# Kernel optimization log

Measured on AMD Instinct MI355X. Metric: run time of the kernel, lower is better.

The kernel has to match this reference:

```python
import jax, jax.numpy as jnp
import numpy as np

N = 50000
E = 800000
IN_DIM = 128
HID = 64
OUT_DIM = 128
NEG_SLOPE = 0.2  # PyG GATConv default


def _add_self_loops(src, dst, edge_attr, n):
    # PyG GATConv(add_self_loops=True) with edge_dim uses fill_value='mean':
    # self-loop edge_attr = mean of edge_attr of incoming edges per node.
    deg = jax.ops.segment_sum(jnp.ones((src.shape[0],), edge_attr.dtype), dst, num_segments=n)
    loop_attr = jax.ops.segment_sum(edge_attr, dst, num_segments=n) / jnp.maximum(deg, 1.0)[:, None]
    loop = jnp.arange(n, dtype=src.dtype)
    return (jnp.concatenate([src, loop]), jnp.concatenate([dst, loop]),
            jnp.concatenate([edge_attr, loop_attr], axis=0))


def _gat_conv(x, src, dst, edge_attr, W, We, a_src, a_dst, a_edge, bias, heads, out_dim, concat, n):
    src, dst, edge_attr = _add_self_loops(src, dst, edge_attr, n)
    h = (x @ W).reshape(n, heads, out_dim)                      # [N,H,D]
    he = (edge_attr @ We).reshape(-1, heads, out_dim)           # [E',H,D]
    alpha_src = jnp.einsum('nhd,hd->nh', h, a_src)
    alpha_dst = jnp.einsum('nhd,hd->nh', h, a_dst)
    alpha_edge = jnp.einsum('ehd,hd->eh', he, a_edge)
    alpha = jax.nn.leaky_relu(alpha_src[src] + alpha_dst[dst] + alpha_edge, NEG_SLOPE)  # [E',H]
    # segment softmax over edges grouped by destination node
    amax = jax.ops.segment_max(alpha, dst, num_segments=n)
    amax = jnp.where(jnp.isfinite(amax), amax, 0.0)
    ex = jnp.exp(alpha - amax[dst])
    denom = jax.ops.segment_sum(ex, dst, num_segments=n)
    coef = ex / (denom[dst] + 1e-16)                            # [E',H]
    msg = h[src] * coef[:, :, None]                             # [E',H,D]
    out = jax.ops.segment_sum(msg, dst, num_segments=n)         # [N,H,D]
    out = out.reshape(n, heads * out_dim) if concat else out.mean(axis=1)
    return out + bias


def setup_inputs() -> dict:
    key = jax.random.key(0)
    ks = jax.random.split(key, 16)
    s = 0.05
    inp = {
        'x': jax.random.normal(ks[0], (N, IN_DIM), jnp.float32),
        'edge_index': jax.random.randint(ks[1], (2, E), 0, N, dtype=jnp.int64),
        'edge_attr': jax.random.normal(ks[2], (E, 2), jnp.float32),
        # gat1: heads=4, concat -> out 4*HID
        'W1': jax.random.normal(ks[3], (IN_DIM, 4 * HID), jnp.float32) * s,
        'We1': jax.random.normal(ks[4], (2, 4 * HID), jnp.float32) * s,
        'asrc1': jax.random.normal(ks[5], (4, HID), jnp.float32) * s,
        'adst1': jax.random.normal(ks[6], (4, HID), jnp.float32) * s,
        'aedge1': jax.random.normal(ks[7], (4, HID), jnp.float32) * s,
        'b1': jnp.zeros((4 * HID,), jnp.float32),
        # gat2: heads=1, concat=False -> out OUT_DIM
        'W2': jax.random.normal(ks[8], (4 * HID, OUT_DIM), jnp.float32) * s,
        'We2': jax.random.normal(ks[9], (2, OUT_DIM), jnp.float32) * s,
        'asrc2': jax.random.normal(ks[10], (1, OUT_DIM), jnp.float32) * s,
        'adst2': jax.random.normal(ks[11], (1, OUT_DIM), jnp.float32) * s,
        'aedge2': jax.random.normal(ks[12], (1, OUT_DIM), jnp.float32) * s,
        'b2': jnp.zeros((OUT_DIM,), jnp.float32),
    }
    return inp


def reference(x, edge_index, edge_attr, W1, We1, asrc1, adst1, aedge1, b1,
              W2, We2, asrc2, adst2, aedge2, b2):
    src, dst = edge_index[0], edge_index[1]
    # dropout layers are identity in eval mode
    h = _gat_conv(x, src, dst, edge_attr, W1, We1, asrc1, adst1, aedge1, b1,
                  heads=4, out_dim=HID, concat=True, n=x.shape[0])
    h = jax.nn.elu(h)
    out = _gat_conv(h, src, dst, edge_attr, W2, We2, asrc2, adst2, aedge2, b2,
                    heads=1, out_dim=OUT_DIM, concat=False, n=x.shape[0])
    return out
```

## Files before the change

### kernel.cpp

```cpp
#include <hip/hip_runtime.h>
#include <hip/hip_bf16.h>

#define NN 50000
#define EE 800000
#define SCAN_B 2048
#define NB ((NN + SCAN_B - 1) / SCAN_B)
#define LOG2E 1.44269504088896340736f


typedef short bf16x8 __attribute__((ext_vector_type(8)));
typedef float f32x4  __attribute__((ext_vector_type(4)));
typedef float f32x2  __attribute__((ext_vector_type(2)));

__device__ __forceinline__ float bf2f(unsigned short u) {
    return __uint_as_float(((unsigned)u) << 16);
}
__device__ __forceinline__ unsigned short f2bf(float f) {
    unsigned b = __float_as_uint(f);
    b += 0x7fffu + ((b >> 16) & 1u);
    return (unsigned short)(b >> 16);
}
__device__ __forceinline__ float2 bfpair(unsigned u) {
    return make_float2(__uint_as_float(u << 16), __uint_as_float(u & 0xffff0000u));
}
__device__ __forceinline__ f32x2 bfpair2(unsigned u) {
    f32x2 r;
    r.x = __uint_as_float(u << 16);
    r.y = __uint_as_float(u & 0xffff0000u);
    return r;
}

__global__ void k_prep(const float* __restrict__ We1, const float* __restrict__ ae1,
                       const float* __restrict__ We2, const float* __restrict__ ae2,
                       float* __restrict__ v,
                       const float* __restrict__ as1, const float* __restrict__ ad1,
                       float* __restrict__ Asd,
                       const float* __restrict__ W1, unsigned short* __restrict__ W1t,
                       const float* __restrict__ W2, unsigned short* __restrict__ W2t,
                       const int* __restrict__ ei, int* __restrict__ idg,
                       int* __restrict__ rank,
                       const float* __restrict__ x, unsigned short* __restrict__ xb) {
    int bid = blockIdx.x, t = threadIdx.x;
    if (bid == 0) {
        if (t < 8) {
            int c = t >> 2, h = t & 3;
            float s = 0.f;
            for (int d = 0; d < 64; d++) s += We1[c * 256 + h * 64 + d] * ae1[h * 64 + d];
            v[c * 4 + h] = s * LOG2E;
        } else if (t < 10) {
            int c = t - 8;
            float s = 0.f;
            for (int d = 0; d < 128; d++) s += We2[c * 128 + d] * ae2[d];
            v[8 + c] = s * LOG2E;
        }
        #pragma unroll 1
        for (int idx = t; idx < 1024; idx += 256) {
            int k = idx >> 3, j = idx & 7;
            const float* a = (j < 4) ? as1 : ad1;
            int h = j & 3;
            float s = 0.f;
            for (int c = 0; c < 64; c++) s += W1[k * 256 + h * 64 + c] * a[h * 64 + c];
            Asd[idx] = s * LOG2E;
        }
    } else if (bid <= 256) {
        int idx = (bid - 1) * 256 + t;
        if (idx < 32768) {
            int k = idx >> 8, n = idx & 255;
            W1t[n * 128 + k] = f2bf(W1[idx]);
        } else {
            int i = idx - 32768;
            int k = i >> 7, n = i & 127;
            W2t[n * 256 + k] = f2bf(W2[i]);
        }
    } else if (bid <= 256 + 3125) {
        int e = (bid - 257) * 256 + t;
        if (e < EE) rank[e] = atomicAdd(&idg[ei[EE + e]], 1);
    } else {
        int i = (bid - 3382) * 256 + t;
        if (i < NN * 128 / 4) {
            float4 vv = ((const float4*)x)[i];
            ushort4 o;
            o.x = f2bf(vv.x); o.y = f2bf(vv.y); o.z = f2bf(vv.z); o.w = f2bf(vv.w);
            ((ushort4*)xb)[i] = o;
        }
    }
}

__global__ void k_scan1(const int* __restrict__ idg, int* __restrict__ rowptr,
                        int* __restrict__ bsum) {
    __shared__ int sh[512];
    int t = threadIdx.x;
    int base = blockIdx.x * SCAN_B + t * 4;
    int v[4]; int s = 0;
    #pragma unroll
    for (int j = 0; j < 4; j++) {
        int i = base + j;
        v[j] = (i < NN) ? idg[i] : 0;
        s += v[j];
    }
    sh[t] = s;
    __syncthreads();
    for (int off = 1; off < 512; off <<= 1) {
        int a = (t >= off) ? sh[t - off] : 0;
        __syncthreads();
        sh[t] += a;
        __syncthreads();
    }
    int run = sh[t] - s;
    #pragma unroll
    for (int j = 0; j < 4; j++) {
        int i = base + j;
        if (i < NN) rowptr[i] = run;
        run += v[j];
    }
    if (t == 511) bsum[blockIdx.x] = sh[511];
}

__global__ void k_scan2(const int* __restrict__ bsum, int* __restrict__ boff,
                        int* __restrict__ rowptr) {
    if (threadIdx.x == 0) {
        int acc = 0;
        for (int b = 0; b < NB; b++) { boff[b] = acc; acc += bsum[b]; }
        rowptr[NN] = acc;
    }
}

__global__ void k_scan3(int* __restrict__ rowptr, const int* __restrict__ boff) {
    int t = threadIdx.x;
    int i = blockIdx.x * SCAN_B + t * 4;
    int off = boff[blockIdx.x];
    #pragma unroll
    for (int j = 0; j < 4; j++)
        if (i + j < NN) rowptr[i + j] += off;
}

__global__ void k_scatter(const int* __restrict__ ei, const float* __restrict__ eattr,
                          const int* __restrict__ rowptr, const int* __restrict__ rank,
                          int2* __restrict__ slot) {
    int e = blockIdx.x * blockDim.x + threadIdx.x;
    if (e >= EE) return;
    int s = ei[e], d = ei[EE + e];
    int p = rowptr[d] + rank[e];
    float2 a = ((const float2*)eattr)[e];
    unsigned a0 = f2bf(a.x), a1 = f2bf(a.y);
    slot[p] = make_int2(s, (int)(a0 | (a1 << 16)));
}

__global__ __launch_bounds__(256) void k_attn1(const unsigned short* __restrict__ xb,
                       const float* __restrict__ Asd,
                       float* __restrict__ asrc, float* __restrict__ adst) {
    int node = blockIdx.x * 4 + (threadIdx.x >> 6);
    if (node >= NN) return;
    int lane = threadIdx.x & 63;
    unsigned xw = *(const unsigned*)(xb + (size_t)node * 128 + lane * 2);
    float2 xc = bfpair(xw);
    const float4* A4 = (const float4*)Asd;
    float4 s0 = A4[lane * 4 + 0];
    float4 d0 = A4[lane * 4 + 1];
    float4 s1 = A4[lane * 4 + 2];
    float4 d1 = A4[lane * 4 + 3];
    float r[8];
    r[0] = xc.x * s0.x + xc.y * s1.x;
    r[1] = xc.x * s0.y + xc.y * s1.y;
    r[2] = xc.x * s0.z + xc.y * s1.z;
    r[3] = xc.x * s0.w + xc.y * s1.w;
    r[4] = xc.x * d0.x + xc.y * d1.x;
    r[5] = xc.x * d0.y + xc.y * d1.y;
    r[6] = xc.x * d0.z + xc.y * d1.z;
    r[7] = xc.x * d0.w + xc.y * d1.w;
    #pragma unroll
    for (int off = 1; off < 64; off <<= 1)
        #pragma unroll
        for (int j = 0; j < 8; j++) r[j] += __shfl_xor(r[j], off);
    if (lane == 0) {
        *(float4*)(asrc + node * 4) = make_float4(r[0], r[1], r[2], r[3]);
        *(float4*)(adst + node * 4) = make_float4(r[4], r[5], r[6], r[7]);
    }
}

__global__ __launch_bounds__(256) void k_agg1x(const int* __restrict__ rowptr,
                       const int2* __restrict__ slot, const float* __restrict__ asrc,
                       const float* __restrict__ adst, const float* __restrict__ v,
                       const unsigned short* __restrict__ xb,
                       unsigned short* __restrict__ Sx) {
    int node = blockIdx.x * 4 + (threadIdx.x >> 6);
    if (node >= NN) return;
    int lane = threadIdx.x & 63;
    int q  = lane >> 4;
    int ql = lane & 15;
    int beg = rowptr[node], end = rowptr[node + 1];
    float4 pd4 = *(const float4*)(adst + node * 4);
    f32x2 pd01 = {pd4.x, pd4.y}, pd23 = {pd4.z, pd4.w};
    f32x2 v001 = {v[0], v[1]},  v023 = {v[2], v[3]};
    f32x2 v101 = {v[4], v[5]},  v123 = {v[6], v[7]};
    f32x2 acc[4][4] = {};
    float den[4] = {};
    float s0 = 0.f, s1 = 0.f;
    const unsigned short* xbq = xb + ql * 8;

    int cnt = end - beg;
    int safeLast = max(end - 1, 0);
    int mend = beg + (cnt & ~3);

    int2 sl0 = slot[min(beg + q, safeLast)];
    int2 sl1 = slot[min(beg + 4 + q, safeLast)];
    float4 as0 = *(const float4*)(asrc + sl0.x * 4);
    uint4  xr0 = *(const uint4*)(xbq + (size_t)sl0.x * 128);

    auto body = [&](int2 cur, float4 cas, uint4 cxr) {
        f32x2 a = bfpair2((unsigned)cur.y);
        f32x2 as01 = {cas.x, cas.y}, as23 = {cas.z, cas.w};
        f32x2 al01 = as01 + pd01 + a.x * v001 + a.y * v101;
        f32x2 al23 = as23 + pd23 + a.x * v023 + a.y * v123;
        float t0 = al01.x, t1 = al01.y, t2 = al23.x, t3 = al23.y;
        t0 = (t0 > 0.f) ? t0 : 0.2f * t0;
        t1 = (t1 > 0.f) ? t1 : 0.2f * t1;
        t2 = (t2 > 0.f) ? t2 : 0.2f * t2;
        t3 = (t3 > 0.f) ? t3 : 0.2f * t3;
        float e0 = __builtin_amdgcn_exp2f(t0);
        float e1 = __builtin_amdgcn_exp2f(t1);
        float e2 = __builtin_amdgcn_exp2f(t2);
        float e3 = __builtin_amdgcn_exp2f(t3);
        den[0] += e0; den[1] += e1; den[2] += e2; den[3] += e3;
        s0 += a.x; s1 += a.y;
        f32x2 xx[4];
        xx[0] = bfpair2(cxr.x); xx[1] = bfpair2(cxr.y);
        xx[2] = bfpair2(cxr.z); xx[3] = bfpair2(cxr.w);
        f32x2 E0 = {e0, e0}, E1 = {e1, e1}, E2 = {e2, e2}, E3 = {e3, e3};
        #pragma unroll
        for (int c = 0; c < 4; c++) {
            acc[0][c] += E0 * xx[c];
            acc[1][c] += E1 * xx[c];
            acc[2][c] += E2 * xx[c];
            acc[3][c] += E3 * xx[c];
        }
    };

    #pragma unroll 2
    for (int pb = beg; pb < mend; pb += 4) {
        int2 cur = sl0; float4 cas = as0; uint4 cxr = xr0;
        sl0 = sl1;
        sl1 = slot[min(pb + 8 + q, safeLast)];
        as0 = *(const float4*)(asrc + sl0.x * 4);
        xr0 = *(const uint4*)(xbq + (size_t)sl0.x * 128);
        body(cur, cas, cxr);
    }
    if (mend + q < end) body(sl0, as0, xr0);

    #pragma unroll
    for (int h = 0; h < 4; h++)
        #pragma unroll
        for (int c = 0; c < 4; c++) {
            acc[h][c].x += __shfl_down(acc[h][c].x, 32);
            acc[h][c].y += __shfl_down(acc[h][c].y, 32);
            acc[h][c].x += __shfl_down(acc[h][c].x, 16);
            acc[h][c].y += __shfl_down(acc[h][c].y, 16);
        }
    #pragma unroll
    for (int h = 0; h < 4; h++) {
        den[h] += __shfl_xor(den[h], 16);
        den[h] += __shfl_xor(den[h], 32);
    }
    s0 += __shfl_xor(s0, 16); s0 += __shfl_xor(s0, 32);
    s1 += __shfl_xor(s1, 16); s1 += __shfl_xor(s1, 32);

    float dg = fmaxf((float)cnt, 1.0f);
    float m0a = s0 / dg, m1a = s1 / dg;
    float4 an4 = *(const float4*)(asrc + node * 4);
    float an[4]  = {an4.x, an4.y, an4.z, an4.w};
    float pdv[4] = {pd01.x, pd01.y, pd23.x, pd23.y};
    float w0[4]  = {v001.x, v001.y, v023.x, v023.y};
    float w1[4]  = {v101.x, v101.y, v123.x, v123.y};
    float exs[4];
    #pragma unroll
    for (int h = 0; h < 4; h++) {
        float als = an[h] + pdv[h] + m0a * w0[h] + m1a * w1[h];
        als = (als > 0.f) ? als : 0.2f * als;
        exs[h] = __builtin_amdgcn_exp2f(als);
        den[h] += exs[h];
    }

    if (q == 0) {
        uint4 r = *(const uint4*)(xbq + (size_t)node * 128);
        f32x2 xs[4] = {bfpair2(r.x), bfpair2(r.y), bfpair2(r.z), bfpair2(r.w)};
        #pragma unroll
        for (int h = 0; h < 4; h++) {
            float inv = 1.f / (den[h] + 1e-16f);
            short ov[8];
            #pragma unroll
            for (int c = 0; c < 4; c++) {
                ov[2 * c]     = (short)f2bf((acc[h][c].x + exs[h] * xs[c].x) * inv);
                ov[2 * c + 1] = (short)f2bf((acc[h][c].y + exs[h] * xs[c].y) * inv);
            }
            bf16x8 o8 = {ov[0], ov[1], ov[2], ov[3], ov[4], ov[5], ov[6], ov[7]};
            *(bf16x8*)(Sx + (size_t)node * 512 + h * 128 + ql * 8) = o8;
        }
    }
}

__global__ __launch_bounds__(256) void k_proj1(const unsigned short* __restrict__ Sx,
                       const unsigned short* __restrict__ W1t,
                       const float* __restrict__ b1,
                       unsigned short* __restrict__ h2b) {
    int h = blockIdx.x;
    int wave = threadIdx.x >> 6, lane = threadIdx.x & 63;
    int l16 = lane & 15, quad = lane >> 4;
    int m0 = blockIdx.y * 128 + wave * 32;

    f32x4 acc[2][4];
    #pragma unroll
    for (int mt = 0; mt < 2; mt++)
        #pragma unroll
        for (int nt = 0; nt < 4; nt++)
            acc[mt][nt] = (f32x4){0.f, 0.f, 0.f, 0.f};

    int ar0 = min(m0 + l16, NN - 1);
    int ar1 = min(m0 + 16 + l16, NN - 1);
    const unsigned short* a0 = Sx + (size_t)ar0 * 512 + h * 128 + quad * 8;
    const unsigned short* a1 = Sx + (size_t)ar1 * 512 + h * 128 + quad * 8;
    const unsigned short* bp = W1t + (size_t)(h * 64 + l16) * 128 + quad * 8;

    #pragma unroll
    for (int k0 = 0; k0 < 128; k0 += 32) {
        bf16x8 af0 = *(const bf16x8*)(a0 + k0);
        bf16x8 af1 = *(const bf16x8*)(a1 + k0);
        #pragma unroll
        for (int nt = 0; nt < 4; nt++) {
            bf16x8 bf = *(const bf16x8*)(bp + (size_t)nt * 16 * 128 + k0);
            acc[0][nt] = __builtin_amdgcn_mfma_f32_16x16x32_bf16(af0, bf, acc[0][nt], 0, 0, 0);
            acc[1][nt] = __builtin_amdgcn_mfma_f32_16x16x32_bf16(af1, bf, acc[1][nt], 0, 0, 0);
        }
    }

    float bia[4];
    #pragma unroll
    for (int nt = 0; nt < 4; nt++) bia[nt] = b1[h * 64 + nt * 16 + l16];

    #pragma unroll
    for (int mt = 0; mt < 2; mt++)
        #pragma unroll
        for (int reg = 0; reg < 4; reg++) {
            int row = m0 + mt * 16 + quad * 4 + reg;
            if (row < NN) {
                #pragma unroll
                for (int nt = 0; nt < 4; nt++) {
                    float va = acc[mt][nt][reg] + bia[nt];
                    va = (va > 0.f) ? va : __expf(va) - 1.f;
                    h2b[(size_t)row * 256 + h * 64 + nt * 16 + l16] = f2bf(va);
                }
            }
        }
}

template <int K, int NT, int H>
__global__ __launch_bounds__(256) void gemm_mfma(const unsigned short* __restrict__ A,
                                                 const unsigned short* __restrict__ Bt,
                                                 unsigned short* __restrict__ C,
                                                 const float* __restrict__ avs,
                                                 const float* __restrict__ avd,
                                                 float* __restrict__ asrc,
                                                 float* __restrict__ adst,
                                                 int M, int N) {
    int wave = threadIdx.x >> 6, lane = threadIdx.x & 63;
    int l16 = lane & 15, quad = lane >> 4;
    int m0 = blockIdx.y * 128 + wave * 32;
    int n0 = blockIdx.x * (NT * 16);

    f32x4 acc[2][NT];
    #pragma unroll
    for (int mt = 0; mt < 2; mt++)
        #pragma unroll
        for (int nt = 0; nt < NT; nt++)
            acc[mt][nt] = (f32x4){0.f, 0.f, 0.f, 0.f};

    int ar0 = min(m0 + l16, M - 1);
    int ar1 = min(m0 + 16 + l16, M - 1);
    const unsigned short* a0 = A + (size_t)ar0 * K + quad * 8;
    const unsigned short* a1 = A + (size_t)ar1 * K + quad * 8;
    const unsigned short* bp = Bt + (size_t)(n0 + l16) * K + quad * 8;

    #pragma unroll
    for (int k0 = 0; k0 < K; k0 += 32) {
        bf16x8 af0 = *(const bf16x8*)(a0 + k0);
        bf16x8 af1 = *(const bf16x8*)(a1 + k0);
        #pragma unroll
        for (int nt = 0; nt < NT; nt++) {
            bf16x8 bf = *(const bf16x8*)(bp + (size_t)nt * 16 * K + k0);
            acc[0][nt] = __builtin_amdgcn_mfma_f32_16x16x32_bf16(af0, bf, acc[0][nt], 0, 0, 0);
            acc[1][nt] = __builtin_amdgcn_mfma_f32_16x16x32_bf16(af1, bf, acc[1][nt], 0, 0, 0);
        }
    }

    #pragma unroll
    for (int mt = 0; mt < 2; mt++)
        #pragma unroll
        for (int reg = 0; reg < 4; reg++) {
            int row = m0 + mt * 16 + quad * 4 + reg;
            if (row < M) {
                #pragma unroll
                for (int nt = 0; nt < NT; nt++)
                    C[(size_t)row * N + n0 + nt * 16 + l16] = f2bf(acc[mt][nt][reg]);
            }
        }

    float ws[NT], wd[NT];
    #pragma unroll
    for (int nt = 0; nt < NT; nt++) {
        ws[nt] = avs[n0 + nt * 16 + l16] * LOG2E;
        wd[nt] = avd[n0 + nt * 16 + l16] * LOG2E;
    }
    int hh = n0 >> 6;
    #pragma unroll
    for (int mt = 0; mt < 2; mt++)
        #pragma unroll
        for (int reg = 0; reg < 4; reg++) {
            int row = m0 + mt * 16 + quad * 4 + reg;
            float s1 = 0.f, s2 = 0.f;
            #pragma unroll
            for (int nt = 0; nt < NT; nt++) {
                float c = acc[mt][nt][reg];
                s1 += c * ws[nt];
                s2 += c * wd[nt];
            }
            #pragma unroll
            for (int off = 1; off < 16; off <<= 1) {
                s1 += __shfl_xor(s1, off);
                s2 += __shfl_xor(s2, off);
            }
            if (l16 == 0 && row < M) {
                asrc[row * H + hh] = s1;
                adst[row * H + hh] = s2;
            }
        }
}

__global__ __launch_bounds__(256) void k_agg2(const int* __restrict__ rowptr,
                       const int2* __restrict__ slot, const float* __restrict__ asrc,
                       const float* __restrict__ adst, const float* __restrict__ v,
                       const unsigned short* __restrict__ gb, const float* __restrict__ b2,
                       float* __restrict__ outp) {
    int node = blockIdx.x * 4 + (threadIdx.x >> 6);
    if (node >= NN) return;
    int lane = threadIdx.x & 63;
    int q  = lane >> 4;
    int ql = lane & 15;
    int beg = rowptr[node], end = rowptr[node + 1];
    float ad = adst[node];
    float v0 = v[0], v1 = v[1];
    f32x2 acc[4] = {};
    float den = 0.f, s0 = 0.f, s1 = 0.f;
    const unsigned short* gbq = gb + ql * 8;

    int cnt = end - beg;
    int safeLast = max(end - 1, 0);
    int mend = beg + (cnt & ~3);

    int2 sl0 = slot[min(beg + q, safeLast)];
    int2 sl1 = slot[min(beg + 4 + q, safeLast)];
    float as0 = asrc[sl0.x];
    uint4 xr0 = *(const uint4*)(gbq + (size_t)sl0.x * 128);

    auto body = [&](int2 cur, float cas, uint4 cxr) {
        f32x2 a = bfpair2((unsigned)cur.y);
        float al = cas + ad + a.x * v0 + a.y * v1;
        al = (al > 0.f) ? al : 0.2f * al;
        float e = __builtin_amdgcn_exp2f(al);
        s0 += a.x; s1 += a.y; den += e;
        f32x2 E = {e, e};
        acc[0] += E * bfpair2(cxr.x);
        acc[1] += E * bfpair2(cxr.y);
        acc[2] += E * bfpair2(cxr.z);
        acc[3] += E * bfpair2(cxr.w);
    };

    #pragma unroll 2
    for (int pb = beg; pb < mend; pb += 4) {
        int2 cur = sl0; float cas = as0; uint4 cxr = xr0;
        sl0 = sl1;
        sl1 = slot[min(pb + 8 + q, safeLast)];
        as0 = asrc[sl0.x];
        xr0 = *(const uint4*)(gbq + (size_t)sl0.x * 128);
        body(cur, cas, cxr);
    }
    if (mend + q < end) body(sl0, as0, xr0);

    #pragma unroll
    for (int k = 0; k < 4; k++) {
        acc[k].x += __shfl_down(acc[k].x, 32);
        acc[k].y += __shfl_down(acc[k].y, 32);
        acc[k].x += __shfl_down(acc[k].x, 16);
        acc[k].y += __shfl_down(acc[k].y, 16);
    }
    den += __shfl_xor(den, 16); den += __shfl_xor(den, 32);
    s0  += __shfl_xor(s0, 16);  s0  += __shfl_xor(s0, 32);
    s1  += __shfl_xor(s1, 16);  s1  += __shfl_xor(s1, 32);

    float dg = fmaxf((float)cnt, 1.0f);
    float als = asrc[node] + ad + (s0 / dg) * v0 + (s1 / dg) * v1;
    als = (als > 0.f) ? als : 0.2f * als;
    float exs = __builtin_amdgcn_exp2f(als);
    den += exs;

    if (q == 0) {
        uint4 r = *(const uint4*)(gbq + (size_t)node * 128);
        f32x2 xs0 = bfpair2(r.x), xs1 = bfpair2(r.y);
        f32x2 xs2 = bfpair2(r.z), xs3 = bfpair2(r.w);
        float inv = 1.f / (den + 1e-16f);
        float4 o0, o1;
        o0.x = (acc[0].x + exs * xs0.x) * inv + b2[ql * 8 + 0];
        o0.y = (acc[0].y + exs * xs0.y) * inv + b2[ql * 8 + 1];
        o0.z = (acc[1].x + exs * xs1.x) * inv + b2[ql * 8 + 2];
        o0.w = (acc[1].y + exs * xs1.y) * inv + b2[ql * 8 + 3];
        o1.x = (acc[2].x + exs * xs2.x) * inv + b2[ql * 8 + 4];
        o1.y = (acc[2].y + exs * xs2.y) * inv + b2[ql * 8 + 5];
        o1.z = (acc[3].x + exs * xs3.x) * inv + b2[ql * 8 + 6];
        o1.w = (acc[3].y + exs * xs3.y) * inv + b2[ql * 8 + 7];
        *(float4*)(outp + (size_t)node * 128 + ql * 8)     = o0;
        *(float4*)(outp + (size_t)node * 128 + ql * 8 + 4) = o1;
    }
}

extern "C" void kernel_launch(void* const* d_in, const int* in_sizes, int n_in,
                              void* d_out, int out_size, void* d_ws, size_t ws_size,
                              hipStream_t stream) {
    const float* x     = (const float*)d_in[0];
    const int*   ei    = (const int*)d_in[1];
    const float* eattr = (const float*)d_in[2];
    const float* W1    = (const float*)d_in[3];
    const float* We1   = (const float*)d_in[4];
    const float* as1   = (const float*)d_in[5];
    const float* ad1   = (const float*)d_in[6];
    const float* ae1   = (const float*)d_in[7];
    const float* b1    = (const float*)d_in[8];
    const float* W2    = (const float*)d_in[9];
    const float* We2   = (const float*)d_in[10];
    const float* as2   = (const float*)d_in[11];
    const float* ad2   = (const float*)d_in[12];
    const float* ae2   = (const float*)d_in[13];
    const float* b2    = (const float*)d_in[14];
    float* out = (float*)d_out;

    int* idg    = (int*)d_ws;
    int* rank   = idg + NN;
    int* rowptr = rank + EE;
    int* bsum   = rowptr + NN + 16;
    int* boff   = bsum + 32;
    int2* slot  = (int2*)(boff + 32);
    float* asrc1 = (float*)(slot + EE);
    float* adst1 = asrc1 + 4 * NN;
    float* asrc2 = adst1 + 4 * NN;
    float* adst2 = asrc2 + NN;
    float* vbuf  = adst2 + NN;
    float* Asd   = vbuf + 64;
    unsigned short* ub = (unsigned short*)(((uintptr_t)(Asd + 1024) + 63) & ~(uintptr_t)63);
    unsigned short* x_bf  = ub;
    unsigned short* W1t   = x_bf + (size_t)NN * 128;
    unsigned short* W2t   = W1t + 32768;
    unsigned short* Sx    = W2t + 32768;
    unsigned short* h2_bf = Sx + (size_t)NN * 512;
    unsigned short* g2_bf = Sx;

    hipMemsetAsync(idg, 0, (size_t)NN * sizeof(int), stream);

    k_prep<<<9632, 256, 0, stream>>>(We1, ae1, We2, ae2, vbuf, as1, ad1, Asd,
                                     W1, W1t, W2, W2t, ei, idg, rank, x, x_bf);
    k_scan1<<<NB, 512, 0, stream>>>(idg, rowptr, bsum);
    k_scan2<<<1, 64, 0, stream>>>(bsum, boff, rowptr);
    k_scan3<<<NB, 512, 0, stream>>>(rowptr, boff);
    k_scatter<<<(EE + 255) / 256, 256, 0, stream>>>(ei, eattr, rowptr, rank, slot);

    k_attn1<<<(NN + 3) / 4, 256, 0, stream>>>(x_bf, Asd, asrc1, adst1);
    k_agg1x<<<(NN + 3) / 4, 256, 0, stream>>>(rowptr, slot, asrc1, adst1, vbuf,
                                              x_bf, Sx);
    k_proj1<<<dim3(4, (NN + 127) / 128), 256, 0, stream>>>(Sx, W1t, b1, h2_bf);

    gemm_mfma<256, 8, 1><<<dim3(1, (NN + 127) / 128), 256, 0, stream>>>(
        h2_bf, W2t, g2_bf, as2, ad2, asrc2, adst2, NN, 128);
    k_agg2<<<(NN + 3) / 4, 256, 0, stream>>>(rowptr, slot, asrc2, adst2, vbuf + 8,
                                             g2_bf, b2, out);
}
```

Baseline: 348.6 us.

## Precompute layer-1 edge exponentials in scatter and deepen gather prefetch pipeline

The layer-1 attention exponentials are now computed per edge inside the CSR scatter kernel, which runs after attn1. They are stored in CSR order in a reused buffer, so the aggregation kernel reads them linearly instead of gathering asrc per neighbour and recomputing exp. Both aggregation kernels also replace the two-deep prefetch loop with a four-slot software pipeline that loads slot indices two groups ahead. This trades an extra 16 B per edge of write plus read, and more registers, for fewer dependent gathers and more memory-level parallelism.

```diff
diff --git a/kernel.cpp b/kernel.cpp
--- a/kernel.cpp
+++ b/kernel.cpp
@@ -134,18 +134,6 @@
         if (i + j < NN) rowptr[i + j] += off;
 }
 
-__global__ void k_scatter(const int* __restrict__ ei, const float* __restrict__ eattr,
-                          const int* __restrict__ rowptr, const int* __restrict__ rank,
-                          int2* __restrict__ slot) {
-    int e = blockIdx.x * blockDim.x + threadIdx.x;
-    if (e >= EE) return;
-    int s = ei[e], d = ei[EE + e];
-    int p = rowptr[d] + rank[e];
-    float2 a = ((const float2*)eattr)[e];
-    unsigned a0 = f2bf(a.x), a1 = f2bf(a.y);
-    slot[p] = make_int2(s, (int)(a0 | (a1 << 16)));
-}
-
 __global__ __launch_bounds__(256) void k_attn1(const unsigned short* __restrict__ xb,
                        const float* __restrict__ Asd,
                        float* __restrict__ asrc, float* __restrict__ adst) {
@@ -178,9 +166,40 @@
     }
 }
 
+__global__ void k_scatter(const int* __restrict__ ei, const float* __restrict__ eattr,
+                          const int* __restrict__ rowptr, const int* __restrict__ rank,
+                          const float* __restrict__ asrc, const float* __restrict__ adst,
+                          const float* __restrict__ v,
+                          int2* __restrict__ slot, float4* __restrict__ e1) {
+    int e = blockIdx.x * blockDim.x + threadIdx.x;
+    if (e >= EE) return;
+    int s = ei[e], d = ei[EE + e];
+    int p = rowptr[d] + rank[e];
+    float2 a = ((const float2*)eattr)[e];
+    unsigned a0 = f2bf(a.x), a1 = f2bf(a.y);
+    slot[p] = make_int2(s, (int)(a0 | (a1 << 16)));
+    float4 s4 = *(const float4*)(asrc + s * 4);
+    float4 d4 = *(const float4*)(adst + d * 4);
+    float al0 = s4.x + d4.x + a.x * v[0] + a.y * v[4];
+    float al1 = s4.y + d4.y + a.x * v[1] + a.y * v[5];
+    float al2 = s4.z + d4.z + a.x * v[2] + a.y * v[6];
+    float al3 = s4.w + d4.w + a.x * v[3] + a.y * v[7];
+    al0 = (al0 > 0.f) ? al0 : 0.2f * al0;
+    al1 = (al1 > 0.f) ? al1 : 0.2f * al1;
+    al2 = (al2 > 0.f) ? al2 : 0.2f * al2;
+    al3 = (al3 > 0.f) ? al3 : 0.2f * al3;
+    float4 ev;
+    ev.x = __builtin_amdgcn_exp2f(al0);
+    ev.y = __builtin_amdgcn_exp2f(al1);
+    ev.z = __builtin_amdgcn_exp2f(al2);
+    ev.w = __builtin_amdgcn_exp2f(al3);
+    e1[p] = ev;
+}
+
 __global__ __launch_bounds__(256) void k_agg1x(const int* __restrict__ rowptr,
-                       const int2* __restrict__ slot, const float* __restrict__ asrc,
-                       const float* __restrict__ adst, const float* __restrict__ v,
+                       const int2* __restrict__ slot, const float* __restrict__ e1v,
+                       const float* __restrict__ asrc, const float* __restrict__ adst,
+                       const float* __restrict__ v,
                        const unsigned short* __restrict__ xb,
                        unsigned short* __restrict__ Sx) {
     int node = blockIdx.x * 4 + (threadIdx.x >> 6);
@@ -189,63 +208,72 @@
     int q  = lane >> 4;
     int ql = lane & 15;
     int beg = rowptr[node], end = rowptr[node + 1];
-    float4 pd4 = *(const float4*)(adst + node * 4);
-    f32x2 pd01 = {pd4.x, pd4.y}, pd23 = {pd4.z, pd4.w};
-    f32x2 v001 = {v[0], v[1]},  v023 = {v[2], v[3]};
-    f32x2 v101 = {v[4], v[5]},  v123 = {v[6], v[7]};
+    int cnt = end - beg;
+    int G = cnt >> 2;
+    int safeLast = max(end - 1, 0);
+    const unsigned short* xbq = xb + ql * 8;
+
     f32x2 acc[4][4] = {};
     float den[4] = {};
     float s0 = 0.f, s1 = 0.f;
-    const unsigned short* xbq = xb + ql * 8;
-
-    int cnt = end - beg;
-    int safeLast = max(end - 1, 0);
-    int mend = beg + (cnt & ~3);
-
-    int2 sl0 = slot[min(beg + q, safeLast)];
-    int2 sl1 = slot[min(beg + 4 + q, safeLast)];
-    float4 as0 = *(const float4*)(asrc + sl0.x * 4);
-    uint4  xr0 = *(const uint4*)(xbq + (size_t)sl0.x * 128);
-
-    auto body = [&](int2 cur, float4 cas, uint4 cxr) {
-        f32x2 a = bfpair2((unsigned)cur.y);
-        f32x2 as01 = {cas.x, cas.y}, as23 = {cas.z, cas.w};
-        f32x2 al01 = as01 + pd01 + a.x * v001 + a.y * v101;
-        f32x2 al23 = as23 + pd23 + a.x * v023 + a.y * v123;
-        float t0 = al01.x, t1 = al01.y, t2 = al23.x, t3 = al23.y;
-        t0 = (t0 > 0.f) ? t0 : 0.2f * t0;
-        t1 = (t1 > 0.f) ? t1 : 0.2f * t1;
-        t2 = (t2 > 0.f) ? t2 : 0.2f * t2;
-        t3 = (t3 > 0.f) ? t3 : 0.2f * t3;
-        float e0 = __builtin_amdgcn_exp2f(t0);
-        float e1 = __builtin_amdgcn_exp2f(t1);
-        float e2 = __builtin_amdgcn_exp2f(t2);
-        float e3 = __builtin_amdgcn_exp2f(t3);
-        den[0] += e0; den[1] += e1; den[2] += e2; den[3] += e3;
-        s0 += a.x; s1 += a.y;
-        f32x2 xx[4];
-        xx[0] = bfpair2(cxr.x); xx[1] = bfpair2(cxr.y);
-        xx[2] = bfpair2(cxr.z); xx[3] = bfpair2(cxr.w);
-        f32x2 E0 = {e0, e0}, E1 = {e1, e1}, E2 = {e2, e2}, E3 = {e3, e3};
-        #pragma unroll
-        for (int c = 0; c < 4; c++) {
-            acc[0][c] += E0 * xx[c];
-            acc[1][c] += E1 * xx[c];
-            acc[2][c] += E2 * xx[c];
-            acc[3][c] += E3 * xx[c];
-        }
-    };
-
-    #pragma unroll 2
-    for (int pb = beg; pb < mend; pb += 4) {
-        int2 cur = sl0; float4 cas = as0; uint4 cxr = xr0;
-        sl0 = sl1;
-        sl1 = slot[min(pb + 8 + q, safeLast)];
-        as0 = *(const float4*)(asrc + sl0.x * 4);
-        xr0 = *(const uint4*)(xbq + (size_t)sl0.x * 128);
-        body(cur, cas, cxr);
-    }
-    if (mend + q < end) body(sl0, as0, xr0);
+
+    int2 r0, r1, r2, r3;
+    int at0, at1, at2, at3;
+    float4 ev0, ev1, ev2, ev3;
+    uint4 xr0, xr1, xr2, xr3;
+
+#define A1_LOADR(K, grp) { \
+    int _i = min(beg + 4 * (grp) + q, safeLast); \
+    r##K = slot[_i]; }
+#define A1_LOADX(K, grp) { \
+    int _i = min(beg + 4 * (grp) + q, safeLast); \
+    at##K = r##K.y; \
+    ev##K = *(const float4*)(e1v + (size_t)_i * 4); \
+    xr##K = *(const uint4*)(xbq + (size_t)(unsigned)r##K.x * 128); }
+#define A1_DO(AT, EV, XR) { \
+    f32x2 a = bfpair2((unsigned)(AT)); \
+    s0 += a.x; s1 += a.y; \
+    den[0] += (EV).x; den[1] += (EV).y; den[2] += (EV).z; den[3] += (EV).w; \
+    f32x2 xx[4]; \
+    xx[0] = bfpair2((XR).x); xx[1] = bfpair2((XR).y); \
+    xx[2] = bfpair2((XR).z); xx[3] = bfpair2((XR).w); \
+    f32x2 E0 = {(EV).x, (EV).x}, E1 = {(EV).y, (EV).y}; \
+    f32x2 E2 = {(EV).z, (EV).z}, E3 = {(EV).w, (EV).w}; \
+    _Pragma("unroll") \
+    for (int c = 0; c < 4; c++) { \
+        acc[0][c] += E0 * xx[c]; acc[1][c] += E1 * xx[c]; \
+        acc[2][c] += E2 * xx[c]; acc[3][c] += E3 * xx[c]; } }
+#define A1_BODY(K) A1_DO(at##K, ev##K, xr##K)
+
+    A1_LOADR(0, 0); A1_LOADR(1, 1); A1_LOADR(2, 2); A1_LOADR(3, 3);
+    A1_LOADX(0, 0); A1_LOADX(1, 1); A1_LOADX(2, 2); A1_LOADX(3, 3);
+    A1_LOADR(0, 4); A1_LOADR(1, 5); A1_LOADR(2, 6); A1_LOADR(3, 7);
+
+    int g = 0;
+    #pragma unroll 1
+    for (; g + 4 <= G; g += 4) {
+        A1_BODY(0); A1_LOADX(0, g + 4); A1_LOADR(0, g + 8);
+        A1_BODY(1); A1_LOADX(1, g + 5); A1_LOADR(1, g + 9);
+        A1_BODY(2); A1_LOADX(2, g + 6); A1_LOADR(2, g + 10);
+        A1_BODY(3); A1_LOADX(3, g + 7); A1_LOADR(3, g + 11);
+    }
+    if (g     < G) { A1_BODY(0); }
+    if (g + 1 < G) { A1_BODY(1); }
+    if (g + 2 < G) { A1_BODY(2); }
+    if (g + 3 < G) { A1_BODY(3); }
+
+    int tail = cnt & 3;
+    if (q < tail) {
+        int _i = beg + 4 * G + q;
+        int2 tl = slot[_i];
+        float4 tev = *(const float4*)(e1v + (size_t)_i * 4);
+        uint4 txr = *(const uint4*)(xbq + (size_t)(unsigned)tl.x * 128);
+        A1_DO(tl.y, tev, txr);
+    }
+#undef A1_LOADR
+#undef A1_LOADX
+#undef A1_DO
+#undef A1_BODY
 
     #pragma unroll
     for (int h = 0; h < 4; h++)
@@ -267,14 +295,13 @@
     float dg = fmaxf((float)cnt, 1.0f);
     float m0a = s0 / dg, m1a = s1 / dg;
     float4 an4 = *(const float4*)(asrc + node * 4);
+    float4 pd4 = *(const float4*)(adst + node * 4);
     float an[4]  = {an4.x, an4.y, an4.z, an4.w};
-    float pdv[4] = {pd01.x, pd01.y, pd23.x, pd23.y};
-    float w0[4]  = {v001.x, v001.y, v023.x, v023.y};
-    float w1[4]  = {v101.x, v101.y, v123.x, v123.y};
+    float pdv[4] = {pd4.x, pd4.y, pd4.z, pd4.w};
     float exs[4];
     #pragma unroll
     for (int h = 0; h < 4; h++) {
-        float als = an[h] + pdv[h] + m0a * w0[h] + m1a * w1[h];
+        float als = an[h] + pdv[h] + m0a * v[h] + m1a * v[4 + h];
         als = (als > 0.f) ? als : 0.2f * als;
         exs[h] = __builtin_amdgcn_exp2f(als);
         den[h] += exs[h];
@@ -445,44 +472,65 @@
     int q  = lane >> 4;
     int ql = lane & 15;
     int beg = rowptr[node], end = rowptr[node + 1];
+    int cnt = end - beg;
+    int G = cnt >> 2;
+    int safeLast = max(end - 1, 0);
     float ad = adst[node];
     float v0 = v[0], v1 = v[1];
     f32x2 acc[4] = {};
     float den = 0.f, s0 = 0.f, s1 = 0.f;
     const unsigned short* gbq = gb + ql * 8;
 
-    int cnt = end - beg;
-    int safeLast = max(end - 1, 0);
-    int mend = beg + (cnt & ~3);
-
-    int2 sl0 = slot[min(beg + q, safeLast)];
-    int2 sl1 = slot[min(beg + 4 + q, safeLast)];
-    float as0 = asrc[sl0.x];
-    uint4 xr0 = *(const uint4*)(gbq + (size_t)sl0.x * 128);
-
-    auto body = [&](int2 cur, float cas, uint4 cxr) {
-        f32x2 a = bfpair2((unsigned)cur.y);
-        float al = cas + ad + a.x * v0 + a.y * v1;
-        al = (al > 0.f) ? al : 0.2f * al;
-        float e = __builtin_amdgcn_exp2f(al);
-        s0 += a.x; s1 += a.y; den += e;
-        f32x2 E = {e, e};
-        acc[0] += E * bfpair2(cxr.x);
-        acc[1] += E * bfpair2(cxr.y);
-        acc[2] += E * bfpair2(cxr.z);
-        acc[3] += E * bfpair2(cxr.w);
-    };
-
-    #pragma unroll 2
-    for (int pb = beg; pb < mend; pb += 4) {
-        int2 cur = sl0; float cas = as0; uint4 cxr = xr0;
-        sl0 = sl1;
-        sl1 = slot[min(pb + 8 + q, safeLast)];
-        as0 = asrc[sl0.x];
-        xr0 = *(const uint4*)(gbq + (size_t)sl0.x * 128);
-        body(cur, cas, cxr);
-    }
-    if (mend + q < end) body(sl0, as0, xr0);
+    int2 r0, r1, r2, r3;
+    int at0, at1, at2, at3;
+    float as0, as1_, as2_, as3;
+    uint4 xr0, xr1, xr2, xr3;
+
+#define A2_LOADR(K, grp) { \
+    int _i = min(beg + 4 * (grp) + q, safeLast); \
+    r##K = slot[_i]; }
+#define A2_LOADX(K, AS) { \
+    at##K = r##K.y; \
+    AS = asrc[r##K.x]; \
+    xr##K = *(const uint4*)(gbq + (size_t)(unsigned)r##K.x * 128); }
+#define A2_DO(AT, AS, XR) { \
+    f32x2 a = bfpair2((unsigned)(AT)); \
+    float al = (AS) + ad + a.x * v0 + a.y * v1; \
+    al = (al > 0.f) ? al : 0.2f * al; \
+    float e = __builtin_amdgcn_exp2f(al); \
+    s0 += a.x; s1 += a.y; den += e; \
+    f32x2 E = {e, e}; \
+    acc[0] += E * bfpair2((XR).x); acc[1] += E * bfpair2((XR).y); \
+    acc[2] += E * bfpair2((XR).z); acc[3] += E * bfpair2((XR).w); }
+
+    A2_LOADR(0, 0); A2_LOADR(1, 1); A2_LOADR(2, 2); A2_LOADR(3, 3);
+    A2_LOADX(0, as0); A2_LOADX(1, as1_); A2_LOADX(2, as2_); A2_LOADX(3, as3);
+    A2_LOADR(0, 4); A2_LOADR(1, 5); A2_LOADR(2, 6); A2_LOADR(3, 7);
+
+    int g = 0;
+    #pragma unroll 1
+    for (; g + 4 <= G; g += 4) {
+        A2_DO(at0, as0, xr0);  A2_LOADX(0, as0);  A2_LOADR(0, g + 8);
+        A2_DO(at1, as1_, xr1); A2_LOADX(1, as1_); A2_LOADR(1, g + 9);
+        A2_DO(at2, as2_, xr2); A2_LOADX(2, as2_); A2_LOADR(2, g + 10);
+        A2_DO(at3, as3, xr3);  A2_LOADX(3, as3);  A2_LOADR(3, g + 11);
+    }
+    if (g     < G) { A2_DO(at0, as0, xr0); }
+    if (g + 1 < G) { A2_DO(at1, as1_, xr1); }
+    if (g + 2 < G) { A2_DO(at2, as2_, xr2); }
+    if (g + 3 < G) { A2_DO(at3, as3, xr3); }
+
+    int tail = cnt & 3;
+    if (q < tail) {
+        int _i = beg + 4 * G + q;
+        int2 tl = slot[_i];
+        float tas = asrc[tl.x];
+        uint4 txr = *(const uint4*)(gbq + (size_t)(unsigned)tl.x * 128);
+        A2_DO(tl.y, tas, txr);
+    }
+#undef A2_LOADR
+#undef A2_LOADX
+#undef A2_DO
 
     #pragma unroll
     for (int k = 0; k < 4; k++) {
@@ -559,6 +607,7 @@
     unsigned short* Sx    = W2t + 32768;
     unsigned short* h2_bf = Sx + (size_t)NN * 512;
     unsigned short* g2_bf = Sx;
+    float4* e1   = (float4*)h2_bf;
 
     hipMemsetAsync(idg, 0, (size_t)NN * sizeof(int), stream);
 
@@ -567,11 +616,12 @@
     k_scan1<<<NB, 512, 0, stream>>>(idg, rowptr, bsum);
     k_scan2<<<1, 64, 0, stream>>>(bsum, boff, rowptr);
     k_scan3<<<NB, 512, 0, stream>>>(rowptr, boff);
-    k_scatter<<<(EE + 255) / 256, 256, 0, stream>>>(ei, eattr, rowptr, rank, slot);
 
     k_attn1<<<(NN + 3) / 4, 256, 0, stream>>>(x_bf, Asd, asrc1, adst1);
-    k_agg1x<<<(NN + 3) / 4, 256, 0, stream>>>(rowptr, slot, asrc1, adst1, vbuf,
-                                              x_bf, Sx);
+    k_scatter<<<(EE + 255) / 256, 256, 0, stream>>>(ei, eattr, rowptr, rank,
+                                                    asrc1, adst1, vbuf, slot, e1);
+    k_agg1x<<<(NN + 3) / 4, 256, 0, stream>>>(rowptr, slot, (const float*)e1,
+                                              asrc1, adst1, vbuf, x_bf, Sx);
     k_proj1<<<dim3(4, (NN + 127) / 128), 256, 0, stream>>>(Sx, W1t, b1, h2_bf);
 
     gemm_mfma<256, 8, 1><<<dim3(1, (NN + 127) / 128), 256, 0, stream>>>(
```

New measurement: 385.0 us. 10.5% more time.
